# Performance work log

Measured on AMD Instinct MI355X. Metric: run time of the kernel, lower is better.

Reference implementation:

```python
import jax, jax.numpy as jnp
import numpy as np

B, D_IN, D_OUT, Q_DIM = 8192, 400, 100, 10


def setup_inputs() -> dict:
    key = jax.random.key(0)
    kx, kw = jax.random.split(key)
    X = jax.random.normal(kx, (B, D_IN, Q_DIM), dtype=jnp.float32)
    # FRMap weight: randn(d_out, d_in) / sqrt(d_in)
    W = jax.random.normal(kw, (D_OUT, D_IN), dtype=jnp.float32) / (D_IN ** 0.5)
    return {"X": X, "W": W}


def reference(X, W):
    # FRMap: Y[b] = W @ X[b]  -> (B, d_out, q)
    Y = jnp.einsum('oi,biq->boq', W, X)
    # ReOrth: reduced QR of each tall-skinny (d_out, q) matrix, keep Q
    Q, _ = jnp.linalg.qr(Y, mode='reduced')  # (B, d_out, q)
    return Q
```

## Files before the change

kernel.cpp:

```cpp
#include <hip/hip_runtime.h>
#include <math.h>

#define BATCHES 8192
#define D_IN    400
#define D_OUT   100
#define QD      10
#define KT      64
#define NKT     7
#define MTILES  7
#define WFSZ    (NKT * MTILES * 2 * 64 * 8)
#define XB      648
#define NW      4
#define WCH     512
#define WHALF   (14 * WCH)

using bf16x8 = __attribute__((ext_vector_type(8))) short;
using f32x4  = __attribute__((ext_vector_type(4))) float;

template <int CTRL>
__device__ __forceinline__ float dpp_add(float x) {
  int s = __builtin_amdgcn_update_dpp(0, __builtin_bit_cast(int, x),
                                      CTRL, 0xF, 0xF, true);
  return x + __builtin_bit_cast(float, s);
}

__device__ __forceinline__ float wsum64(float x) {
  x = dpp_add<0x111>(x);
  x = dpp_add<0x112>(x);
  x = dpp_add<0x114>(x);
  x = dpp_add<0x118>(x);
  x = dpp_add<0x142>(x);
  x = dpp_add<0x143>(x);
  return __builtin_bit_cast(float,
      __builtin_amdgcn_readlane(__builtin_bit_cast(int, x), 63));
}

__device__ __forceinline__ float lane_bcast(float x, int lane) {
  return __builtin_bit_cast(float,
      __builtin_amdgcn_readlane(__builtin_bit_cast(int, x), lane));
}

__device__ __forceinline__ void gload_lds16(const short* g, short* l) {
  __builtin_amdgcn_global_load_lds(
      (const __attribute__((address_space(1))) void*)g,
      (__attribute__((address_space(3))) void*)l, 16, 0, 0);
}

__global__ __launch_bounds__(256) void wprep_kernel(const float* __restrict__ W,
                                                    short* __restrict__ wfh,
                                                    short* __restrict__ wfl) {
  const int e = blockIdx.x * 256 + threadIdx.x;
  if (e >= WFSZ) return;
  const int j = e & 7, lane = (e >> 3) & 63, ks = (e >> 9) & 1, mtkt = e >> 10;
  const int kt = mtkt / MTILES, mt = mtkt - kt * MTILES;
  const int o = mt * 16 + (lane & 15);
  const int k = kt * KT + ks * 32 + (lane >> 4) * 8 + j;
  const float w = (o < D_OUT && k < D_IN) ? W[o * D_IN + k] : 0.f;
  __bf16 h = (__bf16)w;
  float hf = (float)h;
  __bf16 l = (__bf16)(w - hf);
  wfh[e] = __builtin_bit_cast(short, h);
  wfl[e] = __builtin_bit_cast(short, l);
}

__device__ __forceinline__ void qr_and_store(const f32x4* acc, float* stg,
                                             float* dst, int lane, int col,
                                             int quad) {
  if (col < QD) {
    #pragma unroll
    for (int mt = 0; mt < MTILES; ++mt)
      #pragma unroll
      for (int rr = 0; rr < 4; ++rr) {
        const int o = mt * 16 + quad * 4 + rr;
        if (o < D_OUT) stg[o * QD + col] = acc[mt][rr];
      }
  }
  const int r = lane;
  float a0[QD], a1[QD];
  #pragma unroll
  for (int q = 0; q < QD; ++q) a0[q] = stg[r * QD + q];
  const bool has1 = (r + 64) < D_OUT;
  #pragma unroll
  for (int q = 0; q < QD; ++q) a1[q] = has1 ? stg[(r + 64) * QD + q] : 0.f;

  float v0[QD], v1[QD], tau[QD];
  #pragma unroll
  for (int j = 0; j < QD; ++j) {
    float cj0  = (r >= j) ? a0[j] : 0.f;
    float part = cj0 * cj0 + a1[j] * a1[j];
    float sig  = wsum64(part);
    float alpha = lane_bcast(a0[j], j);
    float nrm  = __builtin_amdgcn_sqrtf(sig);
    float aab  = fabsf(alpha);
    float rn   = __builtin_amdgcn_rcpf(nrm);
    float rd   = __builtin_amdgcn_rcpf(aab + nrm);
    float sgn  = (alpha >= 0.f) ? 1.f : -1.f;
    float tj   = (sig > 0.f) ? (1.f + aab * rn) : 0.f;
    float inv  = (sig > 0.f) ? sgn * rd : 0.f;
    tau[j] = tj;
    v0[j]  = (r == j) ? 1.f : ((r > j) ? a0[j] * inv : 0.f);
    v1[j]  = a1[j] * inv;
    #pragma unroll
    for (int k = j + 1; k < QD; ++k) {
      float p = v0[j] * a0[k] + v1[j] * a1[k];
      float s = wsum64(p) * tj;
      a0[k] -= s * v0[j];
      a1[k] -= s * v1[j];
    }
  }
  float q0[QD], q1[QD];
  #pragma unroll
  for (int c = 0; c < QD; ++c) { q0[c] = (r == c) ? 1.f : 0.f; q1[c] = 0.f; }
  #pragma unroll
  for (int j = QD - 1; j >= 0; --j) {
    #pragma unroll
    for (int c = j; c < QD; ++c) {
      float p = v0[j] * q0[c] + v1[j] * q1[c];
      float s = wsum64(p) * tau[j];
      q0[c] -= s * v0[j];
      q1[c] -= s * v1[j];
    }
  }
  #pragma unroll
  for (int c = 0; c < QD; ++c) stg[r * QD + c] = q0[c];
  if (has1) {
    #pragma unroll
    for (int c = 0; c < QD; ++c) stg[(r + 64) * QD + c] = q1[c];
  }
  const float4* src = (const float4*)stg;
  float4* d4 = (float4*)dst;
  #pragma unroll
  for (int u = r; u < (D_OUT * QD) / 4; u += 64) d4[u] = src[u];
}

__global__ __launch_bounds__(256, 3) void fused_kernel(const float* __restrict__ X,
                                                       const short* __restrict__ wfh,
                                                       const short* __restrict__ wfl,
                                                       float* __restrict__ out) {
  __shared__ __align__(16) float xstg[NW * 2 * XB];
  __shared__ __align__(16) short wtile[2 * WHALF];
  const int tid  = threadIdx.x;
  const int lane = tid & 63;
  const int wv   = __builtin_amdgcn_readfirstlane(tid >> 6);
  const long b0  = (long)blockIdx.x * (NW * 2) + wv * 2;
  float* xs = xstg + wv * (2 * XB);
  const int col = lane & 15, quad = lane >> 4;

  f32x4 acc0[MTILES], acc1[MTILES];
  #pragma unroll
  for (int t = 0; t < MTILES; ++t) {
    acc0[t] = (f32x4){0.f, 0.f, 0.f, 0.f};
    acc1[t] = (f32x4){0.f, 0.f, 0.f, 0.f};
  }

  auto wissue = [&](int kt, int ks, int half) {
    #pragma unroll
    for (int i = 0; i < 4; ++i) {
      const int c = wv + 4 * i;
      if (c < 14) {
        const short* pl = (c < 7) ? wfh : wfl;
        const int m = (c < 7) ? c : c - 7;
        gload_lds16(pl + ((long)(kt * MTILES + m) * 2 + ks) * WCH + lane * 8,
                    &wtile[half * WHALF + c * WCH]);
      }
    }
  };

  float4 pre[5];
  auto xpre = [&](int kt) {
    const int nk0 = kt * KT;
    const int vf4 = (nk0 + KT <= D_IN) ? 160 : ((D_IN - nk0) * QD) / 4;
    #pragma unroll
    for (int u = 0; u < 5; ++u) {
      const int idx = lane + u * 64;
      const int bsel = idx >= 160 ? 1 : 0;
      const int within = idx - bsel * 160;
      float4 v = {0.f, 0.f, 0.f, 0.f};
      if (within < vf4)
        v = *(const float4*)(X + (b0 + bsel) * (long)(D_IN * QD) + nk0 * QD + within * 4);
      pre[u] = v;
    }
  };
  auto xcommit = [&]() {
    #pragma unroll
    for (int u = 0; u < 5; ++u) {
      const int idx = lane + u * 64;
      const int bsel = idx >= 160 ? 1 : 0;
      const int within = idx - bsel * 160;
      *(float4*)&xs[bsel * XB + within * 4] = pre[u];
    }
  };

  auto computeHalf = [&](int ks, int half) {
    bf16x8 b0h, b0l, b1h, b1l;
    #pragma unroll
    for (int m = 0; m < 8; ++m) {
      const int fo = (ks * 32 + quad * 8 + m) * QD + col;
      float x0 = xs[fo];
      float x1 = xs[XB + fo];
      __bf16 h0 = (__bf16)x0; float f0 = (float)h0; __bf16 g0 = (__bf16)(x0 - f0);
      __bf16 h1 = (__bf16)x1; float f1 = (float)h1; __bf16 g1 = (__bf16)(x1 - f1);
      b0h[m] = __builtin_bit_cast(short, h0); b0l[m] = __builtin_bit_cast(short, g0);
      b1h[m] = __builtin_bit_cast(short, h1); b1l[m] = __builtin_bit_cast(short, g1);
    }
    const short* wb = &wtile[half * WHALF];
    #pragma unroll
    for (int mt = 0; mt < MTILES; ++mt) {
      bf16x8 ah = *(const bf16x8*)(wb + mt * WCH + lane * 8);
      bf16x8 al = *(const bf16x8*)(wb + (7 + mt) * WCH + lane * 8);
      acc0[mt] = __builtin_amdgcn_mfma_f32_16x16x32_bf16(ah, b0h, acc0[mt], 0, 0, 0);
      acc0[mt] = __builtin_amdgcn_mfma_f32_16x16x32_bf16(al, b0h, acc0[mt], 0, 0, 0);
      acc0[mt] = __builtin_amdgcn_mfma_f32_16x16x32_bf16(ah, b0l, acc0[mt], 0, 0, 0);
      acc1[mt] = __builtin_amdgcn_mfma_f32_16x16x32_bf16(ah, b1h, acc1[mt], 0, 0, 0);
      acc1[mt] = __builtin_amdgcn_mfma_f32_16x16x32_bf16(al, b1h, acc1[mt], 0, 0, 0);
      acc1[mt] = __builtin_amdgcn_mfma_f32_16x16x32_bf16(ah, b1l, acc1[mt], 0, 0, 0);
    }
  };

  wissue(0, 0, 0);
  __builtin_amdgcn_sched_barrier(0);
  xpre(0);
  asm volatile("s_waitcnt vmcnt(5)" ::: "memory");
  __builtin_amdgcn_s_barrier();
  __builtin_amdgcn_sched_barrier(0);

  #pragma unroll 1
  for (int kt = 0; kt < NKT; ++kt) {
    xcommit();
    wissue(kt, 1, 1);
    computeHalf(0, 0);
    asm volatile("s_waitcnt vmcnt(0)" ::: "memory");
    __builtin_amdgcn_s_barrier();
    __builtin_amdgcn_sched_barrier(0);
    if (kt + 1 < NKT) {
      wissue(kt + 1, 0, 0);
      __builtin_amdgcn_sched_barrier(0);
      xpre(kt + 1);
    }
    computeHalf(1, 1);
    if (kt + 1 < NKT) {
      asm volatile("s_waitcnt vmcnt(5)" ::: "memory");
      __builtin_amdgcn_s_barrier();
      __builtin_amdgcn_sched_barrier(0);
    }
  }

  qr_and_store(acc0, xs, out + b0 * (long)(D_OUT * QD), lane, col, quad);
  qr_and_store(acc1, xs, out + (b0 + 1) * (long)(D_OUT * QD), lane, col, quad);
}

extern "C" void kernel_launch(void* const* d_in, const int* in_sizes, int n_in,
                              void* d_out, int out_size, void* d_ws, size_t ws_size,
                              hipStream_t stream) {
  const float* X = (const float*)d_in[0];
  const float* W = (const float*)d_in[1];
  float* out = (float*)d_out;
  short* wfh = (short*)d_ws;
  short* wfl = wfh + WFSZ;
  hipLaunchKernelGGL(wprep_kernel, dim3((WFSZ + 255) / 256), dim3(256), 0, stream,
                     W, wfh, wfl);
  hipLaunchKernelGGL(fused_kernel, dim3(BATCHES / (NW * 2)), dim3(256), 0, stream,
                     X, wfh, wfl, out);
}
```

Before: 220.8 us.

## Split W staging into hi/lo quarter buffers to raise occupancy to four blocks

The shared-memory W tile is halved by staging hi and lo bf16 planes separately in two quarter-sized buffers. X staging per wave is also packed without padding. Together these shrink LDS use so launch bounds can ask for four blocks per CU instead of three. The MFMA loop is split into separate hi and lo passes, which doubles the number of barrier and full vmcnt waits per k-tile. That trades latency hiding within a block for more resident waves.

Result: slower. 258.4 us (+17.0%).

```diff
diff --git a/kernel.cpp b/kernel.cpp
--- a/kernel.cpp
+++ b/kernel.cpp
@@ -9,10 +9,10 @@
 #define NKT     7
 #define MTILES  7
 #define WFSZ    (NKT * MTILES * 2 * 64 * 8)
-#define XB      648
+#define XBW     1280
 #define NW      4
 #define WCH     512
-#define WHALF   (14 * WCH)
+#define QTR     (7 * WCH)
 
 using bf16x8 = __attribute__((ext_vector_type(8))) short;
 using f32x4  = __attribute__((ext_vector_type(4))) float;
@@ -133,17 +133,17 @@
   for (int u = r; u < (D_OUT * QD) / 4; u += 64) d4[u] = src[u];
 }
 
-__global__ __launch_bounds__(256, 3) void fused_kernel(const float* __restrict__ X,
+__global__ __launch_bounds__(256, 4) void fused_kernel(const float* __restrict__ X,
                                                        const short* __restrict__ wfh,
                                                        const short* __restrict__ wfl,
                                                        float* __restrict__ out) {
-  __shared__ __align__(16) float xstg[NW * 2 * XB];
-  __shared__ __align__(16) short wtile[2 * WHALF];
+  __shared__ __align__(16) float xstg[NW * XBW];
+  __shared__ __align__(16) short wtile[2 * QTR];
   const int tid  = threadIdx.x;
   const int lane = tid & 63;
   const int wv   = __builtin_amdgcn_readfirstlane(tid >> 6);
   const long b0  = (long)blockIdx.x * (NW * 2) + wv * 2;
-  float* xs = xstg + wv * (2 * XB);
+  float* xs = xstg + wv * XBW;
   const int col = lane & 15, quad = lane >> 4;
 
   f32x4 acc0[MTILES], acc1[MTILES];
@@ -153,17 +153,13 @@
     acc1[t] = (f32x4){0.f, 0.f, 0.f, 0.f};
   }
 
-  auto wissue = [&](int kt, int ks, int half) {
-    #pragma unroll
-    for (int i = 0; i < 4; ++i) {
-      const int c = wv + 4 * i;
-      if (c < 14) {
-        const short* pl = (c < 7) ? wfh : wfl;
-        const int m = (c < 7) ? c : c - 7;
-        gload_lds16(pl + ((long)(kt * MTILES + m) * 2 + ks) * WCH + lane * 8,
-                    &wtile[half * WHALF + c * WCH]);
-      }
-    }
+  auto wissue = [&](int kt, int ks, const short* pl, int buf) {
+    const int m1 = wv;
+    const int m2 = (wv < 3) ? wv + 4 : 6;
+    gload_lds16(pl + ((long)(kt * MTILES + m1) * 2 + ks) * WCH + lane * 8,
+                &wtile[buf * QTR + m1 * WCH]);
+    gload_lds16(pl + ((long)(kt * MTILES + m2) * 2 + ks) * WCH + lane * 8,
+                &wtile[buf * QTR + m2 * WCH]);
   };
 
   float4 pre[5];
@@ -185,64 +181,77 @@
     #pragma unroll
     for (int u = 0; u < 5; ++u) {
       const int idx = lane + u * 64;
-      const int bsel = idx >= 160 ? 1 : 0;
-      const int within = idx - bsel * 160;
-      *(float4*)&xs[bsel * XB + within * 4] = pre[u];
-    }
-  };
-
-  auto computeHalf = [&](int ks, int half) {
-    bf16x8 b0h, b0l, b1h, b1l;
+      *(float4*)&xs[idx * 4] = pre[u];
+    }
+  };
+
+  bf16x8 b0h, b0l, b1h, b1l;
+  auto buildFrags = [&](int ks) {
     #pragma unroll
     for (int m = 0; m < 8; ++m) {
       const int fo = (ks * 32 + quad * 8 + m) * QD + col;
       float x0 = xs[fo];
-      float x1 = xs[XB + fo];
+      float x1 = xs[640 + fo];
       __bf16 h0 = (__bf16)x0; float f0 = (float)h0; __bf16 g0 = (__bf16)(x0 - f0);
       __bf16 h1 = (__bf16)x1; float f1 = (float)h1; __bf16 g1 = (__bf16)(x1 - f1);
       b0h[m] = __builtin_bit_cast(short, h0); b0l[m] = __builtin_bit_cast(short, g0);
       b1h[m] = __builtin_bit_cast(short, h1); b1l[m] = __builtin_bit_cast(short, g1);
     }
-    const short* wb = &wtile[half * WHALF];
+  };
+  auto computeHi = [&](int buf) {
     #pragma unroll
     for (int mt = 0; mt < MTILES; ++mt) {
-      bf16x8 ah = *(const bf16x8*)(wb + mt * WCH + lane * 8);
-      bf16x8 al = *(const bf16x8*)(wb + (7 + mt) * WCH + lane * 8);
+      bf16x8 ah = *(const bf16x8*)&wtile[buf * QTR + mt * WCH + lane * 8];
       acc0[mt] = __builtin_amdgcn_mfma_f32_16x16x32_bf16(ah, b0h, acc0[mt], 0, 0, 0);
-      acc0[mt] = __builtin_amdgcn_mfma_f32_16x16x32_bf16(al, b0h, acc0[mt], 0, 0, 0);
       acc0[mt] = __builtin_amdgcn_mfma_f32_16x16x32_bf16(ah, b0l, acc0[mt], 0, 0, 0);
       acc1[mt] = __builtin_amdgcn_mfma_f32_16x16x32_bf16(ah, b1h, acc1[mt], 0, 0, 0);
+      acc1[mt] = __builtin_amdgcn_mfma_f32_16x16x32_bf16(ah, b1l, acc1[mt], 0, 0, 0);
+    }
+  };
+  auto computeLo = [&](int buf) {
+    #pragma unroll
+    for (int mt = 0; mt < MTILES; ++mt) {
+      bf16x8 al = *(const bf16x8*)&wtile[buf * QTR + mt * WCH + lane * 8];
+      acc0[mt] = __builtin_amdgcn_mfma_f32_16x16x32_bf16(al, b0h, acc0[mt], 0, 0, 0);
       acc1[mt] = __builtin_amdgcn_mfma_f32_16x16x32_bf16(al, b1h, acc1[mt], 0, 0, 0);
-      acc1[mt] = __builtin_amdgcn_mfma_f32_16x16x32_bf16(ah, b1l, acc1[mt], 0, 0, 0);
-    }
-  };
-
-  wissue(0, 0, 0);
+    }
+  };
+
+  wissue(0, 0, wfh, 0);
   __builtin_amdgcn_sched_barrier(0);
   xpre(0);
-  asm volatile("s_waitcnt vmcnt(5)" ::: "memory");
-  __builtin_amdgcn_s_barrier();
   __builtin_amdgcn_sched_barrier(0);
 
   #pragma unroll 1
   for (int kt = 0; kt < NKT; ++kt) {
     xcommit();
-    wissue(kt, 1, 1);
-    computeHalf(0, 0);
+    buildFrags(0);
     asm volatile("s_waitcnt vmcnt(0)" ::: "memory");
     __builtin_amdgcn_s_barrier();
     __builtin_amdgcn_sched_barrier(0);
-    if (kt + 1 < NKT) {
-      wissue(kt + 1, 0, 0);
-      __builtin_amdgcn_sched_barrier(0);
-      xpre(kt + 1);
-    }
-    computeHalf(1, 1);
-    if (kt + 1 < NKT) {
+    wissue(kt, 0, wfl, 1);
+    computeHi(0);
+    asm volatile("s_waitcnt vmcnt(0)" ::: "memory");
+    __builtin_amdgcn_s_barrier();
+    __builtin_amdgcn_sched_barrier(0);
+    wissue(kt, 1, wfh, 0);
+    computeLo(1);
+    asm volatile("s_waitcnt vmcnt(0)" ::: "memory");
+    __builtin_amdgcn_s_barrier();
+    __builtin_amdgcn_sched_barrier(0);
+    buildFrags(1);
+    wissue(kt, 1, wfl, 1);
+    __builtin_amdgcn_sched_barrier(0);
+    if (kt + 1 < NKT) xpre(kt + 1);
+    computeHi(0);
+    if (kt + 1 < NKT)
       asm volatile("s_waitcnt vmcnt(5)" ::: "memory");
-      __builtin_amdgcn_s_barrier();
-      __builtin_amdgcn_sched_barrier(0);
-    }
+    else
+      asm volatile("s_waitcnt vmcnt(0)" ::: "memory");
+    __builtin_amdgcn_s_barrier();
+    __builtin_amdgcn_sched_barrier(0);
+    if (kt + 1 < NKT) wissue(kt + 1, 0, wfh, 0);
+    computeLo(1);
   }
 
   qr_and_store(acc0, xs, out + b0 * (long)(D_OUT * QD), lane, col, quad);
```
